# Performance work log

Measured on AMD Instinct MI355X. Metric: run time of the kernel, lower is better.

The kernel has to match this reference:

```python
import jax, jax.numpy as jnp
import numpy as np

N = 50000   # total faces (nodes) across batch
E = 800000  # total edges (avg degree 16), assumed to include self-loops
B = 16      # number of graphs in batch
H = 4       # attention heads
D = 64      # per-head dim
HID = H * D # 256
OUT = 512   # brep_dim


def _ln(x, g, b, eps=1e-5):
    mu = x.mean(-1, keepdims=True)
    v = ((x - mu) ** 2).mean(-1, keepdims=True)
    return (x - mu) * jax.lax.rsqrt(v + eps) * g + b


def setup_inputs() -> dict:
    key = jax.random.key(0)
    ks = jax.random.split(key, 32)
    p = lambda i, s: jax.random.normal(ks[i], s, jnp.float32) * 0.05
    inp = {
        'x_face': jax.random.normal(ks[0], (N, 7), jnp.float32),
        'x_edge': jax.random.normal(ks[1], (E, 6), jnp.float32),
        'face_W': p(2, (7, HID)), 'face_b': p(3, (HID,)),
        'face_g': jnp.ones((HID,), jnp.float32), 'face_beta': jnp.zeros((HID,), jnp.float32),
        'edge_W': p(4, (6, HID)), 'edge_b': p(5, (HID,)),
        'edge_g': jnp.ones((HID,), jnp.float32), 'edge_beta': jnp.zeros((HID,), jnp.float32),
        'g0_W': p(6, (HID, HID)), 'g0_al': p(7, (H, D)), 'g0_ar': p(8, (H, D)), 'g0_bias': p(9, (HID,)),
        'g0_g': jnp.ones((HID,), jnp.float32), 'g0_beta': jnp.zeros((HID,), jnp.float32),
        'g1_W': p(10, (HID, HID)), 'g1_al': p(11, (H, D)), 'g1_ar': p(12, (H, D)), 'g1_bias': p(13, (HID,)),
        'g1_g': jnp.ones((HID,), jnp.float32), 'g1_beta': jnp.zeros((HID,), jnp.float32),
        'gate_W': p(14, (HID, 1)), 'gate_b': p(15, (1,)),
        'out_W': p(16, (HID, OUT)), 'out_b': p(17, (OUT,)),
        'out_g': jnp.ones((OUT,), jnp.float32), 'out_beta': jnp.zeros((OUT,), jnp.float32),
        'src': jax.random.randint(ks[18], (E,), 0, N, jnp.int32),
        'dst': jax.random.randint(ks[19], (E,), 0, N, jnp.int32),
        'graph_ids': (jnp.arange(N) // (N // B)).astype(jnp.int32),
        'num_graphs': B,
    }
    return inp


def reference(x_face, x_edge, face_W, face_b, face_g, face_beta,
              edge_W, edge_b, edge_g, edge_beta,
              g0_W, g0_al, g0_ar, g0_bias, g0_g, g0_beta,
              g1_W, g1_al, g1_ar, g1_bias, g1_g, g1_beta,
              gate_W, gate_b, out_W, out_b, out_g, out_beta,
              src, dst, graph_ids, num_graphs):
    n = x_face.shape[0]
    # face / edge encoders: Linear -> ReLU -> LayerNorm (dropout=0 in eval)
    h = _ln(jax.nn.relu(x_face @ face_W + face_b), face_g, face_beta)          # [N,HID]
    eenc = _ln(jax.nn.relu(x_edge @ edge_W + edge_b), edge_g, edge_beta)       # [E,HID]
    # copy_e + mean aggregation onto dst nodes
    cnt = jax.ops.segment_sum(jnp.ones((eenc.shape[0],), eenc.dtype), dst, n)  # [N]
    agg = jax.ops.segment_sum(eenc, dst, n) / jnp.maximum(cnt, 1.0)[:, None]
    h = h + agg

    def gat(h, W, al, ar, bias, g, b):
        f = (h @ W).reshape(n, H, D)                          # [N,H,D]
        el = (f * al).sum(-1)                                 # [N,H]
        er = (f * ar).sum(-1)                                 # [N,H]
        e = jax.nn.leaky_relu(el[src] + er[dst], 0.2)          # [E,H]
        m = jax.ops.segment_max(e, dst, n)                    # edge softmax over in-edges per dst
        ex = jnp.exp(e - m[dst])
        s = jax.ops.segment_sum(ex, dst, n)
        a = ex / s[dst]                                       # [E,H]
        r = jax.ops.segment_sum(f[src] * a[:, :, None], dst, n)  # [N,H,D]
        r = jax.nn.relu(r + bias.reshape(1, H, D)).reshape(n, H * D)
        return _ln(r, g, b)

    h = gat(h, g0_W, g0_al, g0_ar, g0_bias, g0_g, g0_beta)
    h = gat(h, g1_W, g1_al, g1_ar, g1_bias, g1_g, g1_beta)

    # GlobalAttentionPooling: per-graph segment softmax on gate scores
    gate = (h @ gate_W + gate_b)[:, 0]                        # [N]
    gm = jax.ops.segment_max(gate, graph_ids, num_graphs)
    ge = jnp.exp(gate - gm[graph_ids])
    gs = jax.ops.segment_sum(ge, graph_ids, num_graphs)
    w = (ge / gs[graph_ids])[:, None]
    pooled = jax.ops.segment_sum(w * h, graph_ids, num_graphs)  # [B,HID]

    feat = _ln(jax.nn.relu(pooled @ out_W + out_b), out_g, out_beta)  # [B,OUT]
    return feat, h, pooled
```

## Files before the change

### kernel.cpp

```cpp
#include <hip/hip_runtime.h>

#define N_FACES 50000
#define N_EDGES 800000
#define NB      16
#define HID     256
#define NOUT    512
#define SCAN_B  1024
#define SCAN_NB ((N_FACES + SCAN_B - 1) / SCAN_B)
#define NT      (N_FACES / 16)

typedef __attribute__((ext_vector_type(8))) short short8v;
typedef __attribute__((ext_vector_type(4))) float float4v;
union U8 { uint4 u; short8v s; };

__device__ __forceinline__ float wave_sum(float v) {
#pragma unroll
  for (int o = 32; o; o >>= 1) v += __shfl_xor(v, o, 64);
  return v;
}

__device__ __forceinline__ unsigned enc_ord(float v) {
  unsigned b = __float_as_uint(v);
  return (b & 0x80000000u) ? ~b : (b | 0x80000000u);
}
__device__ __forceinline__ float dec_ord(unsigned e) {
  unsigned b = (e & 0x80000000u) ? (e ^ 0x80000000u) : ~e;
  return __uint_as_float(b);
}

__device__ __forceinline__ unsigned f2bf(float x) {
  unsigned u = __float_as_uint(x);
  return (u + 0x7fffu + ((u >> 16) & 1u)) >> 16;
}
__device__ __forceinline__ float bf_lo(unsigned u) { return __uint_as_float(u << 16); }
__device__ __forceinline__ float bf_hi(unsigned u) { return __uint_as_float(u & 0xffff0000u); }

__global__ void k_hist(const int* __restrict__ dst, int* __restrict__ cnt) {
  int e = blockIdx.x * blockDim.x + threadIdx.x;
  if (e < N_EDGES) atomicAdd(&cnt[dst[e]], 1);
}

__global__ void k_scan1(const int* __restrict__ cnt, int* __restrict__ bsum) {
  __shared__ int sh[SCAN_B];
  int i = blockIdx.x * SCAN_B + threadIdx.x;
  sh[threadIdx.x] = (i < N_FACES) ? cnt[i] : 0;
  __syncthreads();
  for (int off = SCAN_B / 2; off; off >>= 1) {
    if (threadIdx.x < off) sh[threadIdx.x] += sh[threadIdx.x + off];
    __syncthreads();
  }
  if (threadIdx.x == 0) bsum[blockIdx.x] = sh[0];
}

__global__ void k_scan2(int* __restrict__ bsum) {
  int t = threadIdx.x;
  int v = (t < SCAN_NB) ? bsum[t] : 0;
  int inc = v;
#pragma unroll
  for (int off = 1; off < 64; off <<= 1) {
    int u = __shfl_up(inc, off, 64);
    if (t >= off) inc += u;
  }
  if (t < SCAN_NB) bsum[t] = inc - v;
}

__global__ void k_scan3(const int* __restrict__ cnt, const int* __restrict__ bsum,
                        int* __restrict__ row_ptr) {
  __shared__ int sh[SCAN_B];
  int i = blockIdx.x * SCAN_B + threadIdx.x;
  int v = (i < N_FACES) ? cnt[i] : 0;
  sh[threadIdx.x] = v;
  __syncthreads();
  for (int off = 1; off < SCAN_B; off <<= 1) {
    int x = (threadIdx.x >= off) ? sh[threadIdx.x - off] : 0;
    __syncthreads();
    sh[threadIdx.x] += x;
    __syncthreads();
  }
  if (i < N_FACES) row_ptr[i] = bsum[blockIdx.x] + sh[threadIdx.x] - v;
  if (i == 0) row_ptr[N_FACES] = N_EDGES;
}

__global__ void k_scatter(const int* __restrict__ dst, const int* __restrict__ src,
                          const float* __restrict__ xe, const int* __restrict__ row_ptr,
                          const float* __restrict__ eW, const float* __restrict__ eB,
                          int* __restrict__ fill, uint4* __restrict__ rec16,
                          int* __restrict__ csr_src) {
  __shared__ float sw[6][HID];
  __shared__ float sb[HID];
  int t = threadIdx.x;
  for (int i = t; i < 6 * HID; i += 256) sw[i / HID][i % HID] = eW[i];
  for (int i = t; i < HID; i += 256) sb[i] = eB[i];
  __syncthreads();

  int e = blockIdx.x * 64 + (t >> 2);
  int seg = t & 3;
  unsigned zb[6];
  float z[6];
#pragma unroll
  for (int k = 0; k < 6; ++k) {
    zb[k] = f2bf(xe[(size_t)e * 6 + k]);
    z[k] = __uint_as_float(zb[k] << 16);
  }
  int pos = 0;
  if (seg == 0) {
    int d = dst[e];
    int p = atomicAdd(&fill[d], 1);
    pos = row_ptr[d] + p;
  }
  pos = __shfl(pos, (t & 63) & ~3, 64);

  float s1 = 0.f, s2 = 0.f;
  int cbase = seg * 64;
  int rot = 4 * seg;
#pragma unroll 4
  for (int ii = 0; ii < 16; ++ii) {
    int c = cbase + ((4 * ii + rot) & 63);
    float4 w4 = *reinterpret_cast<const float4*>(&sb[c]);
#pragma unroll
    for (int k = 0; k < 6; ++k) {
      float4 m4 = *reinterpret_cast<const float4*>(&sw[k][c]);
      w4.x = fmaf(z[k], m4.x, w4.x); w4.y = fmaf(z[k], m4.y, w4.y);
      w4.z = fmaf(z[k], m4.z, w4.z); w4.w = fmaf(z[k], m4.w, w4.w);
    }
    w4.x = fmaxf(w4.x, 0.f); w4.y = fmaxf(w4.y, 0.f);
    w4.z = fmaxf(w4.z, 0.f); w4.w = fmaxf(w4.w, 0.f);
    s1 += (w4.x + w4.y) + (w4.z + w4.w);
    s2 += (w4.x * w4.x + w4.y * w4.y) + (w4.z * w4.z + w4.w * w4.w);
  }
  s1 += __shfl_xor(s1, 1, 64); s1 += __shfl_xor(s1, 2, 64);
  s2 += __shfl_xor(s2, 1, 64); s2 += __shfl_xor(s2, 2, 64);
  if (seg == 0) {
    float mu = s1 * (1.f / HID);
    float rs = rsqrtf(fmaxf(s2 * (1.f / HID) - mu * mu, 0.f) + 1e-5f);
    csr_src[pos] = src[e];
    rec16[pos] = make_uint4(zb[0] | (zb[1] << 16), zb[2] | (zb[3] << 16),
                            zb[4] | (zb[5] << 16), f2bf(mu) | (f2bf(rs) << 16));
  }
}

__global__ void k_encode(const float* __restrict__ xf, const uint4* __restrict__ rec16,
                         const float* __restrict__ fW, const float* __restrict__ fB,
                         const float* __restrict__ fG, const float* __restrict__ fBe,
                         const float* __restrict__ eW, const float* __restrict__ eB,
                         const float* __restrict__ eG, const float* __restrict__ eBe,
                         const int* __restrict__ row_ptr, float* __restrict__ h,
                         unsigned* __restrict__ hbd) {
  int lane = threadIdx.x & 63;
  int n = blockIdx.x * 4 + (threadIdx.x >> 6);
  if (n >= N_FACES) return;

  float x[7];
#pragma unroll
  for (int k = 0; k < 7; ++k) x[k] = xf[n * 7 + k];
  float y[4];
#pragma unroll
  for (int j = 0; j < 4; ++j) {
    int c = lane + 64 * j;
    float a = fB[c];
#pragma unroll
    for (int k = 0; k < 7; ++k) a += x[k] * fW[k * HID + c];
    y[j] = fmaxf(a, 0.f);
  }
  float s = y[0] + y[1] + y[2] + y[3];
  float s2 = y[0] * y[0] + y[1] * y[1] + y[2] * y[2] + y[3] * y[3];
  s = wave_sum(s); s2 = wave_sum(s2);
  float mu = s * (1.f / HID);
  float rs = rsqrtf(fmaxf(s2 * (1.f / HID) - mu * mu, 0.f) + 1e-5f);
  float hv[4];
#pragma unroll
  for (int j = 0; j < 4; ++j) {
    int c = lane + 64 * j;
    hv[j] = (y[j] - mu) * rs * fG[c] + fBe[c];
  }

  float ew[6][4], eb[4], eg[4], ebe[4];
#pragma unroll
  for (int j = 0; j < 4; ++j) {
    int c = lane + 64 * j;
    eb[j] = eB[c]; eg[j] = eG[c]; ebe[j] = eBe[c];
#pragma unroll
    for (int k = 0; k < 6; ++k) ew[k][j] = eW[k * HID + c];
  }

  int e0 = row_ptr[n], e1 = row_ptr[n + 1];
  float acc[4] = {0.f, 0.f, 0.f, 0.f};
  uint4 pf;
  if (e0 < e1) pf = rec16[e0];
  for (int t = e0; t < e1; ++t) {
    uint4 cu = pf;
    if (t + 1 < e1) pf = rec16[t + 1];
    float z0 = bf_lo(cu.x), z1 = bf_hi(cu.x), z2 = bf_lo(cu.y), z3 = bf_hi(cu.y);
    float z4 = bf_lo(cu.z), z5 = bf_hi(cu.z);
    float emu = bf_lo(cu.w), ers = bf_hi(cu.w);
#pragma unroll
    for (int j = 0; j < 4; ++j) {
      float a = eb[j];
      a = fmaf(z0, ew[0][j], a); a = fmaf(z1, ew[1][j], a);
      a = fmaf(z2, ew[2][j], a); a = fmaf(z3, ew[3][j], a);
      a = fmaf(z4, ew[4][j], a); a = fmaf(z5, ew[5][j], a);
      a = fmaxf(a, 0.f);
      acc[j] += (a - emu) * (ers * eg[j]) + ebe[j];
    }
  }
  float inv = (e1 > e0) ? 1.f / (float)(e1 - e0) : 0.f;
  float hval[4];
#pragma unroll
  for (int j = 0; j < 4; ++j) {
    hval[j] = hv[j] + acc[j] * inv;
    h[(size_t)n * HID + lane + 64 * j] = hval[j];
  }
#pragma unroll
  for (int j = 0; j < 4; ++j) {
    float other = __shfl_xor(hval[j], 1, 64);
    if (!(lane & 1))
      hbd[(size_t)n * 128 + 32 * j + (lane >> 1)] = f2bf(hval[j]) | (f2bf(other) << 16);
  }
}

__global__ void k_packW(const float* __restrict__ W, uint4* __restrict__ Wp) {
  int i = blockIdx.x * 256 + threadIdx.x;
  int lane = i & 63, ks = (i >> 6) & 7, ct = i >> 9;
  int kbase = ks * 32 + (lane >> 4) * 8;
  int col = ct * 16 + (lane & 15);
  unsigned d[4];
#pragma unroll
  for (int r = 0; r < 4; ++r) {
    unsigned lo = f2bf(W[(size_t)(kbase + 2 * r) * HID + col]);
    unsigned hi = f2bf(W[(size_t)(kbase + 2 * r + 1) * HID + col]);
    d[r] = lo | (hi << 16);
  }
  Wp[i] = make_uint4(d[0], d[1], d[2], d[3]);
}

__global__ void k_gemm_mfma(const unsigned* __restrict__ hbd, const uint4* __restrict__ Wp,
                            const float* __restrict__ al, const float* __restrict__ ar,
                            unsigned* __restrict__ fb, float* __restrict__ el,
                            float* __restrict__ er) {
  int tile = blockIdx.x * 4 + (threadIdx.x >> 6);
  if (tile >= NT) return;
  int lane = threadIdx.x & 63;
  int c = lane & 15;
  int kg = lane >> 4;
  int n0 = tile * 16;

  uint4 afrag[8];
#pragma unroll
  for (int ks = 0; ks < 8; ++ks)
    afrag[ks] = *reinterpret_cast<const uint4*>(hbd + (size_t)(n0 + c) * 128 + ks * 16 + kg * 4);

  float4v acc[16];
#pragma unroll
  for (int ct = 0; ct < 16; ++ct) acc[ct] = (float4v){0.f, 0.f, 0.f, 0.f};
#pragma unroll
  for (int ct = 0; ct < 16; ++ct) {
#pragma unroll
    for (int ks = 0; ks < 8; ++ks) {
      U8 a, b;
      a.u = afrag[ks];
      b.u = Wp[(ct * 8 + ks) * 64 + lane];
      acc[ct] = __builtin_amdgcn_mfma_f32_16x16x32_bf16(a.s, b.s, acc[ct], 0, 0, 0);
    }
  }

#pragma unroll
  for (int ct = 0; ct < 16; ++ct) {
#pragma unroll
    for (int reg = 0; reg < 4; ++reg) {
      float v = acc[ct][reg];
      float vo = __shfl_xor(v, 1, 64);
      if (!(lane & 1)) {
        int nd = n0 + kg * 4 + reg;
        fb[(size_t)nd * 128 + ct * 8 + (c >> 1)] = f2bf(v) | (f2bf(vo) << 16);
      }
    }
  }

  float alr[16], arr[16];
#pragma unroll
  for (int ct = 0; ct < 16; ++ct) {
    alr[ct] = al[ct * 16 + c];
    arr[ct] = ar[ct * 16 + c];
  }
#pragma unroll
  for (int hd = 0; hd < 4; ++hd) {
#pragma unroll
    for (int reg = 0; reg < 4; ++reg) {
      float pl = 0.f, pr = 0.f;
#pragma unroll
      for (int q = 0; q < 4; ++q) {
        int ct = hd * 4 + q;
        pl = fmaf(acc[ct][reg], alr[ct], pl);
        pr = fmaf(acc[ct][reg], arr[ct], pr);
      }
#pragma unroll
      for (int o = 1; o < 16; o <<= 1) {
        pl += __shfl_xor(pl, o, 64);
        pr += __shfl_xor(pr, o, 64);
      }
      if (c == 0) {
        int nd = n0 + kg * 4 + reg;
        el[nd * 4 + hd] = pl;
        er[nd * 4 + hd] = pr;
      }
    }
  }
}

__global__ void k_gat(const unsigned* __restrict__ fb, const float* __restrict__ el,
                      const float* __restrict__ er, const int* __restrict__ row_ptr,
                      const int* __restrict__ csrc,
                      const float* __restrict__ bias, const float* __restrict__ g,
                      const float* __restrict__ be, float* __restrict__ h,
                      unsigned* __restrict__ hbd,
                      const float* __restrict__ gw, const float* __restrict__ gb,
                      float* __restrict__ gate) {
  int lane = threadIdx.x & 63;
  int n = blockIdx.x * 4 + (threadIdx.x >> 6);
  if (n >= N_FACES) return;
  int e0 = row_ptr[n], e1 = row_ptr[n + 1];
  float4 ern = reinterpret_cast<const float4*>(er)[n];
  int hh = lane >> 5;
  float ernA = hh ? ern.y : ern.x;
  float ernB = hh ? ern.w : ern.z;

  float sA = 0.f, sB = 0.f;
  float aA0 = 0.f, aA1 = 0.f, aB0 = 0.f, aB1 = 0.f;
  if (e0 < e1) {
    int sp = csrc[e0];
    float4 ep = reinterpret_cast<const float4*>(el)[sp];
    unsigned u0 = fb[(size_t)sp * 128 + lane];
    unsigned u1 = fb[(size_t)sp * 128 + 64 + lane];
    for (int t = e0; t < e1; ++t) {
      float4 ec = ep; unsigned v0 = u0, v1 = u1;
      if (t + 1 < e1) {
        int sn = csrc[t + 1];
        ep = reinterpret_cast<const float4*>(el)[sn];
        u0 = fb[(size_t)sn * 128 + lane];
        u1 = fb[(size_t)sn * 128 + 64 + lane];
      }
      float elA = hh ? ec.y : ec.x;
      float elB = hh ? ec.w : ec.z;
      float w, pA, pB;
      w = elA + ernA; w = fmaxf(w, 0.2f * w); pA = __expf(w); sA += pA;
      w = elB + ernB; w = fmaxf(w, 0.2f * w); pB = __expf(w); sB += pB;
      aA0 = fmaf(__uint_as_float(v0 << 16), pA, aA0);
      aA1 = fmaf(__uint_as_float(v0 & 0xffff0000u), pA, aA1);
      aB0 = fmaf(__uint_as_float(v1 << 16), pB, aB0);
      aB1 = fmaf(__uint_as_float(v1 & 0xffff0000u), pB, aB1);
    }
  }
  float iA = sA > 0.f ? 1.f / sA : 0.f;
  float iB = sB > 0.f ? 1.f / sB : 0.f;
  int c0 = 2 * lane, c2 = 128 + 2 * lane;
  float2 bb0 = *reinterpret_cast<const float2*>(bias + c0);
  float2 bb2 = *reinterpret_cast<const float2*>(bias + c2);
  float y0 = fmaxf(aA0 * iA + bb0.x, 0.f);
  float y1 = fmaxf(aA1 * iA + bb0.y, 0.f);
  float y2 = fmaxf(aB0 * iB + bb2.x, 0.f);
  float y3 = fmaxf(aB1 * iB + bb2.y, 0.f);
  float s = y0 + y1 + y2 + y3;
  float q = y0 * y0 + y1 * y1 + y2 * y2 + y3 * y3;
  s = wave_sum(s); q = wave_sum(q);
  float mu = s * (1.f / HID);
  float rs = rsqrtf(fmaxf(q * (1.f / HID) - mu * mu, 0.f) + 1e-5f);
  float2 gg0 = *reinterpret_cast<const float2*>(g + c0);
  float2 gg2 = *reinterpret_cast<const float2*>(g + c2);
  float2 ee0 = *reinterpret_cast<const float2*>(be + c0);
  float2 ee2 = *reinterpret_cast<const float2*>(be + c2);
  float h0 = (y0 - mu) * rs * gg0.x + ee0.x;
  float h1 = (y1 - mu) * rs * gg0.y + ee0.y;
  float h2 = (y2 - mu) * rs * gg2.x + ee2.x;
  float h3 = (y3 - mu) * rs * gg2.y + ee2.y;
  size_t base = (size_t)n * HID;
  *reinterpret_cast<float2*>(h + base + c0) = make_float2(h0, h1);
  *reinterpret_cast<float2*>(h + base + c2) = make_float2(h2, h3);

  if (hbd) {
    hbd[(size_t)n * 128 + lane] = f2bf(h0) | (f2bf(h1) << 16);
    hbd[(size_t)n * 128 + 64 + lane] = f2bf(h2) | (f2bf(h3) << 16);
  }
  if (gw) {
    float2 w0 = *reinterpret_cast<const float2*>(gw + c0);
    float2 w2 = *reinterpret_cast<const float2*>(gw + c2);
    float p = h0 * w0.x + h1 * w0.y + h2 * w2.x + h3 * w2.y;
    p = wave_sum(p);
    if (lane == 0) gate[n] = p + gb[0];
  }
}

__global__ void k_gmax(const float* __restrict__ gate, const int* __restrict__ gid,
                       unsigned* __restrict__ gmax_u) {
  __shared__ unsigned sm[NB];
  int t = threadIdx.x;
  if (t < NB) sm[t] = 0u;
  __syncthreads();
  int n = blockIdx.x * blockDim.x + t;
  if (n < N_FACES) atomicMax(&sm[gid[n]], enc_ord(gate[n]));
  __syncthreads();
  if (t < NB && sm[t] != 0u) atomicMax(&gmax_u[t], sm[t]);
}

#define PCHUNK 125
__global__ void k_psum(const float* __restrict__ h, const float* __restrict__ gate,
                       const int* __restrict__ gid, const unsigned* __restrict__ gmax_u,
                       float* __restrict__ praw, float* __restrict__ gs) {
  int t = threadIdx.x;
  int n0 = blockIdx.x * PCHUNK;
  int n1 = n0 + PCHUNK;
  if (n1 > N_FACES) n1 = N_FACES;
  if (n0 >= N_FACES) return;
  int cur = gid[n0];
  float gm = dec_ord(gmax_u[cur]);
  float acc = 0.f, wsum = 0.f;
  for (int n = n0; n < n1; ++n) {
    int g = gid[n];
    if (g != cur) {
      atomicAdd(&praw[cur * HID + t], acc);
      if (t == 0) atomicAdd(&gs[cur], wsum);
      acc = 0.f; wsum = 0.f; cur = g; gm = dec_ord(gmax_u[cur]);
    }
    float w = __expf(gate[n] - gm);
    acc += w * h[(size_t)n * HID + t];
    wsum += w;
  }
  atomicAdd(&praw[cur * HID + t], acc);
  if (t == 0) atomicAdd(&gs[cur], wsum);
}

__global__ void k_poolnorm(const float* __restrict__ praw, const float* __restrict__ gs,
                           float* __restrict__ pooled) {
  int b = blockIdx.x, c = threadIdx.x;
  pooled[b * HID + c] = praw[b * HID + c] / gs[b];
}

__global__ void k_out(const float* __restrict__ pooled, const float* __restrict__ oW,
                      const float* __restrict__ oB, const float* __restrict__ oG,
                      const float* __restrict__ oBe, float* __restrict__ feat) {
  int b = blockIdx.x;
  int o = threadIdx.x;
  int lane = o & 63, wid = o >> 6;
  __shared__ float p[HID];
  __shared__ float partS[8], partQ[8];
  __shared__ float shMu, shRs;
  if (o < HID) p[o] = pooled[b * HID + o];
  __syncthreads();
  float a = oB[o];
  for (int k = 0; k < HID; ++k) a += p[k] * oW[k * NOUT + o];
  float y = fmaxf(a, 0.f);
  float s = wave_sum(y), q = wave_sum(y * y);
  if (lane == 0) { partS[wid] = s; partQ[wid] = q; }
  __syncthreads();
  if (o == 0) {
    float S = 0.f, Q = 0.f;
#pragma unroll
    for (int i = 0; i < 8; ++i) { S += partS[i]; Q += partQ[i]; }
    float mu = S * (1.f / NOUT);
    shMu = mu;
    shRs = rsqrtf(fmaxf(Q * (1.f / NOUT) - mu * mu, 0.f) + 1e-5f);
  }
  __syncthreads();
  feat[b * NOUT + o] = (y - shMu) * shRs * oG[o] + oBe[o];
}

extern "C" void kernel_launch(void* const* d_in, const int* in_sizes, int n_in,
                              void* d_out, int out_size, void* d_ws, size_t ws_size,
                              hipStream_t stream) {
  (void)in_sizes; (void)n_in; (void)out_size; (void)ws_size;
  const float* x_face    = (const float*)d_in[0];
  const float* x_edge    = (const float*)d_in[1];
  const float* face_W    = (const float*)d_in[2];
  const float* face_b    = (const float*)d_in[3];
  const float* face_g    = (const float*)d_in[4];
  const float* face_beta = (const float*)d_in[5];
  const float* edge_W    = (const float*)d_in[6];
  const float* edge_b    = (const float*)d_in[7];
  const float* edge_g    = (const float*)d_in[8];
  const float* edge_beta = (const float*)d_in[9];
  const float* g0_W      = (const float*)d_in[10];
  const float* g0_al     = (const float*)d_in[11];
  const float* g0_ar     = (const float*)d_in[12];
  const float* g0_bias   = (const float*)d_in[13];
  const float* g0_g      = (const float*)d_in[14];
  const float* g0_beta   = (const float*)d_in[15];
  const float* g1_W      = (const float*)d_in[16];
  const float* g1_al     = (const float*)d_in[17];
  const float* g1_ar     = (const float*)d_in[18];
  const float* g1_bias   = (const float*)d_in[19];
  const float* g1_g      = (const float*)d_in[20];
  const float* g1_beta   = (const float*)d_in[21];
  const float* gate_W    = (const float*)d_in[22];
  const float* gate_b    = (const float*)d_in[23];
  const float* out_W     = (const float*)d_in[24];
  const float* out_b     = (const float*)d_in[25];
  const float* out_g     = (const float*)d_in[26];
  const float* out_beta  = (const float*)d_in[27];
  const int*   src       = (const int*)d_in[28];
  const int*   dst       = (const int*)d_in[29];
  const int*   gid       = (const int*)d_in[30];

  char* ws = (char*)d_ws;
  size_t off = 0;
  auto take = [&](size_t bytes) -> char* {
    char* pp = ws + off;
    off += (bytes + 255) & ~(size_t)255;
    return pp;
  };
  int*      cnt      = (int*)take((size_t)N_FACES * 4);
  int*      fill     = (int*)take((size_t)N_FACES * 4);
  int*      row_ptr  = (int*)take((size_t)(N_FACES + 1) * 4);
  int*      bsum     = (int*)take((size_t)SCAN_NB * 4);
  int*      csr_src  = (int*)take((size_t)N_EDGES * 4);
  uint4*    rec16    = (uint4*)take((size_t)N_EDGES * 16);
  uint4*    Wp0      = (uint4*)take((size_t)8192 * 16);
  uint4*    Wp1      = (uint4*)take((size_t)8192 * 16);
  unsigned* gmax_u   = (unsigned*)take(64);
  float*    gs       = (float*)take(64);
  float*    praw     = (float*)take((size_t)NB * HID * 4);
  float*    el       = (float*)take((size_t)N_FACES * 4 * 4);
  float*    er       = (float*)take((size_t)N_FACES * 4 * 4);
  float*    gate     = (float*)take((size_t)N_FACES * 4);
  unsigned* fbuf     = (unsigned*)take((size_t)N_FACES * 128 * 4);
  unsigned* hbd      = (unsigned*)take((size_t)N_FACES * 128 * 4);

  float* outp   = (float*)d_out;
  float* feat   = outp;
  float* h      = outp + NB * NOUT;
  float* pooled = outp + NB * NOUT + (size_t)N_FACES * HID;

  hipMemsetAsync(cnt, 0, (size_t)N_FACES * 4, stream);
  hipMemsetAsync(fill, 0, (size_t)N_FACES * 4, stream);
  hipMemsetAsync(gmax_u, 0, 64, stream);
  hipMemsetAsync(gs, 0, 64, stream);
  hipMemsetAsync(praw, 0, (size_t)NB * HID * 4, stream);

  k_hist<<<(N_EDGES + 255) / 256, 256, 0, stream>>>(dst, cnt);
  k_scan1<<<SCAN_NB, SCAN_B, 0, stream>>>(cnt, bsum);
  k_scan2<<<1, 64, 0, stream>>>(bsum);
  k_scan3<<<SCAN_NB, SCAN_B, 0, stream>>>(cnt, bsum, row_ptr);
  k_packW<<<32, 256, 0, stream>>>(g0_W, Wp0);
  k_packW<<<32, 256, 0, stream>>>(g1_W, Wp1);
  k_scatter<<<N_EDGES / 64, 256, 0, stream>>>(dst, src, x_edge, row_ptr,
                                              edge_W, edge_b, fill, rec16, csr_src);

  k_encode<<<N_FACES / 4, 256, 0, stream>>>(x_face, rec16, face_W, face_b, face_g, face_beta,
                                            edge_W, edge_b, edge_g, edge_beta,
                                            row_ptr, h, hbd);
  k_gemm_mfma<<<(NT + 3) / 4, 256, 0, stream>>>(hbd, Wp0, g0_al, g0_ar, fbuf, el, er);
  k_gat<<<N_FACES / 4, 256, 0, stream>>>(fbuf, el, er, row_ptr, csr_src,
                                         g0_bias, g0_g, g0_beta, h, hbd,
                                         nullptr, nullptr, nullptr);
  k_gemm_mfma<<<(NT + 3) / 4, 256, 0, stream>>>(hbd, Wp1, g1_al, g1_ar, fbuf, el, er);
  k_gat<<<N_FACES / 4, 256, 0, stream>>>(fbuf, el, er, row_ptr, csr_src,
                                         g1_bias, g1_g, g1_beta, h, nullptr,
                                         gate_W, gate_b, gate);
  k_gmax<<<(N_FACES + 255) / 256, 256, 0, stream>>>(gate, gid, gmax_u);
  k_psum<<<(N_FACES + PCHUNK - 1) / PCHUNK, 256, 0, stream>>>(h, gate, gid, gmax_u, praw, gs);
  k_poolnorm<<<NB, HID, 0, stream>>>(praw, gs, pooled);
  k_out<<<NB, NOUT, 0, stream>>>(pooled, out_W, out_b, out_g, out_beta, feat);
}
```

Baseline: 539.8 us.

## Sort nodes by in-degree for balanced waves and deepen gather prefetch

Adds a counting sort of nodes by in-degree, capped at 63, producing a permutation that the encode and GAT kernels use to pick which node each wavefront handles. Blocks then hold nodes of similar degree, which is meant to cut load imbalance among the four waves of a block. The edge and GAT gather loops now prefetch two edges ahead instead of one, to hide more memory latency. The edge-LayerNorm mean is folded algebraically into post-loop terms to save per-edge ALU work, and the pooling loop prefetches the next row. The cost is three extra small kernels with atomics, more registers, and node writes scattered in sorted order.

```diff
diff --git a/kernel.cpp b/kernel.cpp
--- a/kernel.cpp
+++ b/kernel.cpp
@@ -79,6 +79,30 @@
   }
   if (i < N_FACES) row_ptr[i] = bsum[blockIdx.x] + sh[threadIdx.x] - v;
   if (i == 0) row_ptr[N_FACES] = N_EDGES;
+}
+
+__global__ void k_dhist(const int* __restrict__ cnt, int* __restrict__ dbin) {
+  int n = blockIdx.x * blockDim.x + threadIdx.x;
+  if (n < N_FACES) atomicAdd(&dbin[min(cnt[n], 63)], 1);
+}
+__global__ void k_dscan(int* __restrict__ dbin) {
+  int t = threadIdx.x;
+  int v = dbin[t];
+  int inc = v;
+#pragma unroll
+  for (int off = 1; off < 64; off <<= 1) {
+    int u = __shfl_up(inc, off, 64);
+    if (t >= off) inc += u;
+  }
+  dbin[t] = inc - v;
+}
+__global__ void k_dscatter(const int* __restrict__ cnt, int* __restrict__ dbin,
+                           int* __restrict__ nperm) {
+  int n = blockIdx.x * blockDim.x + threadIdx.x;
+  if (n < N_FACES) {
+    int p = atomicAdd(&dbin[min(cnt[n], 63)], 1);
+    nperm[p] = n;
+  }
 }
 
 __global__ void k_scatter(const int* __restrict__ dst, const int* __restrict__ src,
@@ -144,11 +168,10 @@
                          const float* __restrict__ fG, const float* __restrict__ fBe,
                          const float* __restrict__ eW, const float* __restrict__ eB,
                          const float* __restrict__ eG, const float* __restrict__ eBe,
-                         const int* __restrict__ row_ptr, float* __restrict__ h,
-                         unsigned* __restrict__ hbd) {
+                         const int* __restrict__ row_ptr, const int* __restrict__ nperm,
+                         float* __restrict__ h, unsigned* __restrict__ hbd) {
   int lane = threadIdx.x & 63;
-  int n = blockIdx.x * 4 + (threadIdx.x >> 6);
-  if (n >= N_FACES) return;
+  int n = nperm[blockIdx.x * 4 + (threadIdx.x >> 6)];
 
   float x[7];
 #pragma unroll
@@ -185,14 +208,18 @@
 
   int e0 = row_ptr[n], e1 = row_ptr[n + 1];
   float acc[4] = {0.f, 0.f, 0.f, 0.f};
-  uint4 pf;
-  if (e0 < e1) pf = rec16[e0];
+  float smu = 0.f;
+  uint4 p0 = {}, p1 = {};
+  if (e0 < e1) p0 = rec16[e0];
+  if (e0 + 1 < e1) p1 = rec16[e0 + 1];
   for (int t = e0; t < e1; ++t) {
-    uint4 cu = pf;
-    if (t + 1 < e1) pf = rec16[t + 1];
+    uint4 cu = p0;
+    p0 = p1;
+    if (t + 2 < e1) p1 = rec16[t + 2];
     float z0 = bf_lo(cu.x), z1 = bf_hi(cu.x), z2 = bf_lo(cu.y), z3 = bf_hi(cu.y);
     float z4 = bf_lo(cu.z), z5 = bf_hi(cu.z);
     float emu = bf_lo(cu.w), ers = bf_hi(cu.w);
+    smu = fmaf(emu, ers, smu);
 #pragma unroll
     for (int j = 0; j < 4; ++j) {
       float a = eb[j];
@@ -200,14 +227,16 @@
       a = fmaf(z2, ew[2][j], a); a = fmaf(z3, ew[3][j], a);
       a = fmaf(z4, ew[4][j], a); a = fmaf(z5, ew[5][j], a);
       a = fmaxf(a, 0.f);
-      acc[j] += (a - emu) * (ers * eg[j]) + ebe[j];
-    }
-  }
-  float inv = (e1 > e0) ? 1.f / (float)(e1 - e0) : 0.f;
+      acc[j] = fmaf(a, ers, acc[j]);
+    }
+  }
+  int cntE = e1 - e0;
+  float inv = (cntE > 0) ? 1.f / (float)cntE : 0.f;
   float hval[4];
 #pragma unroll
   for (int j = 0; j < 4; ++j) {
-    hval[j] = hv[j] + acc[j] * inv;
+    float add = (cntE > 0) ? inv * eg[j] * (acc[j] - smu) + ebe[j] : 0.f;
+    hval[j] = hv[j] + add;
     h[(size_t)n * HID + lane + 64 * j] = hval[j];
   }
 #pragma unroll
@@ -309,15 +338,14 @@
 
 __global__ void k_gat(const unsigned* __restrict__ fb, const float* __restrict__ el,
                       const float* __restrict__ er, const int* __restrict__ row_ptr,
-                      const int* __restrict__ csrc,
+                      const int* __restrict__ csrc, const int* __restrict__ nperm,
                       const float* __restrict__ bias, const float* __restrict__ g,
                       const float* __restrict__ be, float* __restrict__ h,
                       unsigned* __restrict__ hbd,
                       const float* __restrict__ gw, const float* __restrict__ gb,
                       float* __restrict__ gate) {
   int lane = threadIdx.x & 63;
-  int n = blockIdx.x * 4 + (threadIdx.x >> 6);
-  if (n >= N_FACES) return;
+  int n = nperm[blockIdx.x * 4 + (threadIdx.x >> 6)];
   int e0 = row_ptr[n], e1 = row_ptr[n + 1];
   float4 ern = reinterpret_cast<const float4*>(er)[n];
   int hh = lane >> 5;
@@ -326,29 +354,40 @@
 
   float sA = 0.f, sB = 0.f;
   float aA0 = 0.f, aA1 = 0.f, aB0 = 0.f, aB1 = 0.f;
+  const float4* el4 = reinterpret_cast<const float4*>(el);
+  float4 ep1 = {}, ep2 = {};
+  unsigned u10 = 0, u11 = 0, u20 = 0, u21 = 0;
   if (e0 < e1) {
     int sp = csrc[e0];
-    float4 ep = reinterpret_cast<const float4*>(el)[sp];
-    unsigned u0 = fb[(size_t)sp * 128 + lane];
-    unsigned u1 = fb[(size_t)sp * 128 + 64 + lane];
-    for (int t = e0; t < e1; ++t) {
-      float4 ec = ep; unsigned v0 = u0, v1 = u1;
-      if (t + 1 < e1) {
-        int sn = csrc[t + 1];
-        ep = reinterpret_cast<const float4*>(el)[sn];
-        u0 = fb[(size_t)sn * 128 + lane];
-        u1 = fb[(size_t)sn * 128 + 64 + lane];
-      }
-      float elA = hh ? ec.y : ec.x;
-      float elB = hh ? ec.w : ec.z;
-      float w, pA, pB;
-      w = elA + ernA; w = fmaxf(w, 0.2f * w); pA = __expf(w); sA += pA;
-      w = elB + ernB; w = fmaxf(w, 0.2f * w); pB = __expf(w); sB += pB;
-      aA0 = fmaf(__uint_as_float(v0 << 16), pA, aA0);
-      aA1 = fmaf(__uint_as_float(v0 & 0xffff0000u), pA, aA1);
-      aB0 = fmaf(__uint_as_float(v1 << 16), pB, aB0);
-      aB1 = fmaf(__uint_as_float(v1 & 0xffff0000u), pB, aB1);
-    }
+    ep1 = el4[sp];
+    u10 = fb[(size_t)sp * 128 + lane];
+    u11 = fb[(size_t)sp * 128 + 64 + lane];
+  }
+  if (e0 + 1 < e1) {
+    int sp = csrc[e0 + 1];
+    ep2 = el4[sp];
+    u20 = fb[(size_t)sp * 128 + lane];
+    u21 = fb[(size_t)sp * 128 + 64 + lane];
+  }
+  for (int t = e0; t < e1; ++t) {
+    float4 ec = ep1;
+    unsigned v0 = u10, v1 = u11;
+    ep1 = ep2; u10 = u20; u11 = u21;
+    if (t + 2 < e1) {
+      int sn = csrc[t + 2];
+      ep2 = el4[sn];
+      u20 = fb[(size_t)sn * 128 + lane];
+      u21 = fb[(size_t)sn * 128 + 64 + lane];
+    }
+    float elA = hh ? ec.y : ec.x;
+    float elB = hh ? ec.w : ec.z;
+    float w, pA, pB;
+    w = elA + ernA; w = fmaxf(w, 0.2f * w); pA = __expf(w); sA += pA;
+    w = elB + ernB; w = fmaxf(w, 0.2f * w); pB = __expf(w); sB += pB;
+    aA0 = fmaf(__uint_as_float(v0 << 16), pA, aA0);
+    aA1 = fmaf(__uint_as_float(v0 & 0xffff0000u), pA, aA1);
+    aB0 = fmaf(__uint_as_float(v1 << 16), pB, aB0);
+    aB1 = fmaf(__uint_as_float(v1 & 0xffff0000u), pB, aB1);
   }
   float iA = sA > 0.f ? 1.f / sA : 0.f;
   float iB = sB > 0.f ? 1.f / sB : 0.f;
@@ -413,16 +452,24 @@
   int cur = gid[n0];
   float gm = dec_ord(gmax_u[cur]);
   float acc = 0.f, wsum = 0.f;
+  float hc = h[(size_t)n0 * HID + t];
+  float gc = gate[n0];
   for (int n = n0; n < n1; ++n) {
+    float hnext = 0.f, gnext = 0.f;
+    if (n + 1 < n1) {
+      hnext = h[(size_t)(n + 1) * HID + t];
+      gnext = gate[n + 1];
+    }
     int g = gid[n];
     if (g != cur) {
       atomicAdd(&praw[cur * HID + t], acc);
       if (t == 0) atomicAdd(&gs[cur], wsum);
       acc = 0.f; wsum = 0.f; cur = g; gm = dec_ord(gmax_u[cur]);
     }
-    float w = __expf(gate[n] - gm);
-    acc += w * h[(size_t)n * HID + t];
+    float w = __expf(gc - gm);
+    acc += w * hc;
     wsum += w;
+    hc = hnext; gc = gnext;
   }
   atomicAdd(&praw[cur * HID + t], acc);
   if (t == 0) atomicAdd(&gs[cur], wsum);
@@ -510,6 +557,8 @@
   int*      fill     = (int*)take((size_t)N_FACES * 4);
   int*      row_ptr  = (int*)take((size_t)(N_FACES + 1) * 4);
   int*      bsum     = (int*)take((size_t)SCAN_NB * 4);
+  int*      dbin     = (int*)take(64 * 4);
+  int*      nperm    = (int*)take((size_t)N_FACES * 4);
   int*      csr_src  = (int*)take((size_t)N_EDGES * 4);
   uint4*    rec16    = (uint4*)take((size_t)N_EDGES * 16);
   uint4*    Wp0      = (uint4*)take((size_t)8192 * 16);
@@ -530,6 +579,7 @@
 
   hipMemsetAsync(cnt, 0, (size_t)N_FACES * 4, stream);
   hipMemsetAsync(fill, 0, (size_t)N_FACES * 4, stream);
+  hipMemsetAsync(dbin, 0, 64 * 4, stream);
   hipMemsetAsync(gmax_u, 0, 64, stream);
   hipMemsetAsync(gs, 0, 64, stream);
   hipMemsetAsync(praw, 0, (size_t)NB * HID * 4, stream);
@@ -538,6 +588,9 @@
   k_scan1<<<SCAN_NB, SCAN_B, 0, stream>>>(cnt, bsum);
   k_scan2<<<1, 64, 0, stream>>>(bsum);
   k_scan3<<<SCAN_NB, SCAN_B, 0, stream>>>(cnt, bsum, row_ptr);
+  k_dhist<<<(N_FACES + 255) / 256, 256, 0, stream>>>(cnt, dbin);
+  k_dscan<<<1, 64, 0, stream>>>(dbin);
+  k_dscatter<<<(N_FACES + 255) / 256, 256, 0, stream>>>(cnt, dbin, nperm);
   k_packW<<<32, 256, 0, stream>>>(g0_W, Wp0);
   k_packW<<<32, 256, 0, stream>>>(g1_W, Wp1);
   k_scatter<<<N_EDGES / 64, 256, 0, stream>>>(dst, src, x_edge, row_ptr,
@@ -545,13 +598,13 @@
 
   k_encode<<<N_FACES / 4, 256, 0, stream>>>(x_face, rec16, face_W, face_b, face_g, face_beta,
                                             edge_W, edge_b, edge_g, edge_beta,
-                                            row_ptr, h, hbd);
+                                            row_ptr, nperm, h, hbd);
   k_gemm_mfma<<<(NT + 3) / 4, 256, 0, stream>>>(hbd, Wp0, g0_al, g0_ar, fbuf, el, er);
-  k_gat<<<N_FACES / 4, 256, 0, stream>>>(fbuf, el, er, row_ptr, csr_src,
+  k_gat<<<N_FACES / 4, 256, 0, stream>>>(fbuf, el, er, row_ptr, csr_src, nperm,
                                          g0_bias, g0_g, g0_beta, h, hbd,
                                          nullptr, nullptr, nullptr);
   k_gemm_mfma<<<(NT + 3) / 4, 256, 0, stream>>>(hbd, Wp1, g1_al, g1_ar, fbuf, el, er);
-  k_gat<<<N_FACES / 4, 256, 0, stream>>>(fbuf, el, er, row_ptr, csr_src,
+  k_gat<<<N_FACES / 4, 256, 0, stream>>>(fbuf, el, er, row_ptr, csr_src, nperm,
                                          g1_bias, g1_g, g1_beta, h, nullptr,
                                          gate_W, gate_b, gate);
   k_gmax<<<(N_FACES + 255) / 256, 256, 0, stream>>>(gate, gid, gmax_u);
```

After: 800.3 us. +48.3%, slower.
